# Kernel optimization log

Measured on AMD Instinct MI355X. Metric: run time of the kernel, lower is better.

## Reference

```python
import jax, jax.numpy as jnp
import numpy as np

DIM = 768
HEADS = 12
HEAD_DIM = DIM // HEADS


def setup_inputs() -> dict:
    key = jax.random.key(0)
    ks = jax.random.split(key, 5)
    B, S = 4, 2048
    init = 0.02
    x = jax.random.normal(ks[0], (B, S, DIM), dtype=jnp.float32)
    w_qkv = jax.random.normal(ks[1], (DIM, 3 * DIM), dtype=jnp.float32) * init
    b_qkv = jnp.zeros((3 * DIM,), dtype=jnp.float32)
    w_out = jax.random.normal(ks[2], (DIM, DIM), dtype=jnp.float32) * init
    b_out = jnp.zeros((DIM,), dtype=jnp.float32)
    return {"x": x, "w_qkv": w_qkv, "b_qkv": b_qkv, "w_out": w_out, "b_out": b_out}


def reference(x, w_qkv, b_qkv, w_out, b_out):
    B, S, D = x.shape
    # QKV projection: [B,S,3D] -> [3,B,H,S,hd]
    qkv = x @ w_qkv + b_qkv
    qkv = qkv.reshape(B, S, 3, HEADS, HEAD_DIM).transpose(2, 0, 3, 1, 4)
    q, k, v = qkv[0], qkv[1], qkv[2]
    # NOTE: original scales by 1/sqrt(head_num), not 1/sqrt(head_dim)
    scale = 1.0 / jnp.sqrt(jnp.float32(HEADS))
    scores = jnp.einsum("bhqd,bhkd->bhqk", q, k) * scale
    attn = jax.nn.softmax(scores, axis=-1)
    out = jnp.einsum("bhqk,bhkd->bhqd", attn, v)
    out = out.transpose(0, 2, 1, 3).reshape(B, S, D)
    return out @ w_out + b_out
```

## Files before the change

### kernel.cpp

```cpp
#include <hip/hip_runtime.h>
#include <hip/hip_bf16.h>
#include <cstdint>
#include <cstddef>

#define HEADS 12
#define HD    64
#define NB    4
#define SEQ   2048
#define DIM   768
#define NQKV  2304

static constexpr float QSCALE = 0.2886751345948129f * 1.4426950408889634f;

typedef __attribute__((ext_vector_type(8))) short short8;
typedef __attribute__((ext_vector_type(4))) short short4v;
typedef __attribute__((ext_vector_type(4))) float f32x4;

__device__ inline unsigned short f2bf(float x) {
    union { float f; uint32_t u; } v; v.f = x;
    return (unsigned short)((v.u + 0x7fffu + ((v.u >> 16) & 1u)) >> 16);
}

__device__ inline unsigned short f2bf_fast(float x) {
    __hip_bfloat16 h = __float2bfloat16(x);
    unsigned short u;
    __builtin_memcpy(&u, &h, 2);
    return u;
}

__device__ inline void gld16(const void* g, void* l) {
    __builtin_amdgcn_global_load_lds(
        (const __attribute__((address_space(1))) unsigned int*)g,
        (__attribute__((address_space(3))) unsigned int*)l, 16, 0, 0);
}

__global__ __launch_bounds__(256) void convert_x_kernel(
    const float* __restrict__ x, unsigned short* __restrict__ xb)
{
    const size_t i = ((size_t)blockIdx.x * 256 + threadIdx.x) * 8;
    const float4 a = *reinterpret_cast<const float4*>(x + i);
    const float4 b = *reinterpret_cast<const float4*>(x + i + 4);
    short8 o;
    o[0] = (short)f2bf(a.x); o[1] = (short)f2bf(a.y);
    o[2] = (short)f2bf(a.z); o[3] = (short)f2bf(a.w);
    o[4] = (short)f2bf(b.x); o[5] = (short)f2bf(b.y);
    o[6] = (short)f2bf(b.z); o[7] = (short)f2bf(b.w);
    *reinterpret_cast<short8*>(xb + i) = o;
}

__global__ __launch_bounds__(256) void transpose_w_kernel(
    const float* __restrict__ w, unsigned short* __restrict__ wT,
    int ncols , int nrows )
{
    __shared__ float tile[64][65];
    const int k0 = blockIdx.y * 64;
    const int n0 = blockIdx.x * 64;
    const int tr = threadIdx.x >> 4;
    const int tc4 = (threadIdx.x & 15) * 4;
    #pragma unroll
    for (int it = 0; it < 4; ++it) {
        const int kk = tr + it * 16;
        *reinterpret_cast<float4*>(&tile[kk][tc4]) =
            *reinterpret_cast<const float4*>(w + (size_t)(k0 + kk) * ncols + n0 + tc4);
    }
    __syncthreads();
    #pragma unroll
    for (int it = 0; it < 4; ++it) {
        const int nn = tr + it * 16;
        short4v o;
        #pragma unroll
        for (int r = 0; r < 4; ++r) o[r] = (short)f2bf(tile[tc4 + r][nn]);
        *reinterpret_cast<short4v*>(wT + (size_t)(n0 + nn) * nrows + k0 + tc4) = o;
    }
}

__global__ __launch_bounds__(256) void qkv_gemm_bf16(
    const unsigned short* __restrict__ A,
    const unsigned short* __restrict__ BT,
    const float* __restrict__ bias,
    unsigned short* __restrict__ qb, unsigned short* __restrict__ kb,
    unsigned short* __restrict__ vt)
{
    __shared__ __align__(16) unsigned short As[128][64];
    __shared__ __align__(16) unsigned short Bs[128][64];

    const int tid = threadIdx.x;
    const int wave = tid >> 6;
    const int lane = tid & 63;
    const int col = lane & 15;
    const int g = lane >> 4;
    const int m0 = blockIdx.y * 128;
    const int n0 = blockIdx.x * 128;
    const int wr = wave >> 1, wc = wave & 1;

    const int srow = tid >> 3;
    const int scl  = tid & 7;

    f32x4 acc[4][4] = {};

    for (int kt = 0; kt < DIM; kt += 64) {
        __syncthreads();
        #pragma unroll
        for (int it = 0; it < 4; ++it) {
            const int row = srow + it * 32;
            const int cg = scl ^ (row & 7);
            gld16(A + (size_t)(m0 + row) * DIM + kt + cg * 8,
                  &As[0][0] + (size_t)(it * 256 + wave * 64) * 8);
            gld16(BT + (size_t)(n0 + row) * DIM + kt + cg * 8,
                  &Bs[0][0] + (size_t)(it * 256 + wave * 64) * 8);
        }
        __syncthreads();

        #pragma unroll
        for (int ks = 0; ks < 2; ++ks) {
            short8 af[4], bf[4];
            #pragma unroll
            for (int i = 0; i < 4; ++i) {
                const int ra = wr * 64 + i * 16 + col;
                af[i] = *reinterpret_cast<const short8*>(
                    &As[ra][(((ks * 4 + g) ^ (ra & 7)) << 3)]);
                const int rb = wc * 64 + i * 16 + col;
                bf[i] = *reinterpret_cast<const short8*>(
                    &Bs[rb][(((ks * 4 + g) ^ (rb & 7)) << 3)]);
            }
            #pragma unroll
            for (int i = 0; i < 4; ++i)
                #pragma unroll
                for (int j = 0; j < 4; ++j)
                    acc[i][j] = __builtin_amdgcn_mfma_f32_16x16x32_bf16(
                        af[i], bf[j], acc[i][j], 0, 0, 0);
        }
    }

    const int which = n0 / DIM;
    #pragma unroll
    for (int j = 0; j < 4; ++j) {
        const int n = n0 + wc * 64 + j * 16 + col;
        const int rem = n - which * DIM;
        const int h = rem >> 6, dh = rem & 63;
        const float bj = bias[n];
        #pragma unroll
        for (int i = 0; i < 4; ++i) {
            const int mbase = m0 + wr * 64 + i * 16 + g * 4;
            const int b_ = mbase >> 11;
            const int s_ = mbase & 2047;
            const size_t bh = (size_t)(b_ * HEADS + h);
            if (which == 2) {
                short4v pk;
                #pragma unroll
                for (int r = 0; r < 4; ++r)
                    pk[r] = (short)f2bf(acc[i][j][r] + bj);
                *reinterpret_cast<short4v*>(vt + (bh * HD + dh) * SEQ + s_) = pk;
            } else {
                unsigned short* dst = (which == 0) ? qb : kb;
                const float sc = (which == 0) ? QSCALE : 1.0f;
                #pragma unroll
                for (int r = 0; r < 4; ++r)
                    dst[(bh * SEQ + s_ + r) * HD + dh] =
                        f2bf((acc[i][j][r] + bj) * sc);
            }
        }
    }
}

__global__ __launch_bounds__(512) void attn_kernel(
    const unsigned short* __restrict__ qb, const unsigned short* __restrict__ kbuf,
    const unsigned short* __restrict__ vt, unsigned short* __restrict__ ctxb)
{
    __shared__ __align__(16) unsigned short Ks[2][64][64];
    __shared__ __align__(16) unsigned short Vs[2][64][64];
    __shared__ __align__(16) unsigned short Ps[8][16][64];

    const int tid = threadIdx.x;
    const int wave = tid >> 6;
    const int lane = tid & 63;
    const int col = lane & 15;
    const int g   = lane >> 4;

    const int bid = blockIdx.x;
    const int vbid = (bid & 7) * 96 + (bid >> 3);
    const int bh = vbid >> 4;
    const int q0 = (vbid & 15) * 128;
    const int wq = q0 + wave * 16 + col;

    const size_t hb = (size_t)bh * SEQ * HD;

    short8 qf[2];
    {
        const unsigned short* src = qb + hb + (size_t)wq * HD + g * 8;
        qf[0] = *reinterpret_cast<const short8*>(src);
        qf[1] = *reinterpret_cast<const short8*>(src + 32);
    }

    f32x4 acc4[4] = {};
    float l_part = 0.0f;

    const unsigned short* Kg = kbuf + hb;
    const unsigned short* Vg = vt + hb;

    const int srow = tid >> 3;
    const int scl  = tid & 7;
    const int scg  = scl ^ (srow & 7);

    auto STAGE = [&](int jt, int bsel) {
        const int kb0 = jt * 64;
        gld16(Kg + (size_t)(kb0 + srow) * HD + scg * 8,
              &Ks[bsel][0][0] + (size_t)tid * 8);
        gld16(Vg + (size_t)srow * SEQ + kb0 + scg * 8,
              &Vs[bsel][0][0] + (size_t)tid * 8);
    };

    const int NT = SEQ / 64;
    STAGE(0, 0);

    for (int jt = 0; jt < NT; ++jt) {
        const int cur = jt & 1;
        if (jt + 1 < NT) {
            STAGE(jt + 1, cur ^ 1);
            asm volatile("s_waitcnt vmcnt(2)" ::: "memory");
        } else {
            asm volatile("s_waitcnt vmcnt(0)" ::: "memory");
        }
        __builtin_amdgcn_s_barrier();

        f32x4 st[4] = {};
        __builtin_amdgcn_s_setprio(1);
        #pragma unroll
        for (int m = 0; m < 4; ++m) {
            const int row = m * 16 + col;
            const short8 kf0 = *reinterpret_cast<const short8*>(
                &Ks[cur][row][((g ^ (row & 7)) << 3)]);
            const short8 kf1 = *reinterpret_cast<const short8*>(
                &Ks[cur][row][(((g + 4) ^ (row & 7)) << 3)]);
            st[m] = __builtin_amdgcn_mfma_f32_16x16x32_bf16(kf0, qf[0], st[m], 0, 0, 0);
            st[m] = __builtin_amdgcn_mfma_f32_16x16x32_bf16(kf1, qf[1], st[m], 0, 0, 0);
        }
        __builtin_amdgcn_s_setprio(0);

        float s0 = 0.0f, s1 = 0.0f, s2 = 0.0f, s3 = 0.0f;
        #pragma unroll
        for (int m = 0; m < 4; ++m) {
            float p[4];
            p[0] = __builtin_amdgcn_exp2f(st[m][0]);
            p[1] = __builtin_amdgcn_exp2f(st[m][1]);
            p[2] = __builtin_amdgcn_exp2f(st[m][2]);
            p[3] = __builtin_amdgcn_exp2f(st[m][3]);
            s0 += p[0]; s1 += p[1]; s2 += p[2]; s3 += p[3];
            short4v pk;
            #pragma unroll
            for (int r = 0; r < 4; ++r) pk[r] = (short)f2bf_fast(p[r]);
            const int scw = (2 * m + (g >> 1)) ^ (col & 7);
            *reinterpret_cast<short4v*>(
                &Ps[wave][col][(scw << 3) + ((g & 1) << 2)]) = pk;
        }
        l_part += (s0 + s1) + (s2 + s3);

        const short8 pf0 = *reinterpret_cast<const short8*>(
            &Ps[wave][col][((g ^ (col & 7)) << 3)]);
        const short8 pf1 = *reinterpret_cast<const short8*>(
            &Ps[wave][col][(((g + 4) ^ (col & 7)) << 3)]);

        __builtin_amdgcn_s_setprio(1);
        #pragma unroll
        for (int nb = 0; nb < 4; ++nb) {
            const int row = nb * 16 + col;
            const short8 vf0 = *reinterpret_cast<const short8*>(
                &Vs[cur][row][((g ^ (row & 7)) << 3)]);
            const short8 vf1 = *reinterpret_cast<const short8*>(
                &Vs[cur][row][(((g + 4) ^ (row & 7)) << 3)]);
            acc4[nb] = __builtin_amdgcn_mfma_f32_16x16x32_bf16(pf0, vf0, acc4[nb], 0, 0, 0);
            acc4[nb] = __builtin_amdgcn_mfma_f32_16x16x32_bf16(pf1, vf1, acc4[nb], 0, 0, 0);
        }
        __builtin_amdgcn_s_setprio(0);

        __builtin_amdgcn_s_barrier();
    }

    float lt = l_part + __shfl_xor(l_part, 16);
    lt += __shfl_xor(lt, 32);
    float lr[4];
    #pragma unroll
    for (int r = 0; r < 4; ++r) lr[r] = 1.0f / __shfl(lt, g * 4 + r);
    const int b_ = bh / HEADS;
    const int h = bh - b_ * HEADS;
    #pragma unroll
    for (int nb = 0; nb < 4; ++nb)
        #pragma unroll
        for (int r = 0; r < 4; ++r) {
            const int s_ = q0 + wave * 16 + g * 4 + r;
            ctxb[((size_t)b_ * SEQ + s_) * DIM + h * HD + nb * 16 + col] =
                f2bf_fast(acc4[nb][r] * lr[r]);
        }
}

__global__ __launch_bounds__(256) void out_gemm_bf16(
    const unsigned short* __restrict__ A,
    const unsigned short* __restrict__ BT,
    const float* __restrict__ bias, float* __restrict__ out)
{
    __shared__ __align__(16) unsigned short As[128][64];
    __shared__ __align__(16) unsigned short Bs[128][64];

    const int tid = threadIdx.x;
    const int wave = tid >> 6;
    const int lane = tid & 63;
    const int col = lane & 15;
    const int g = lane >> 4;
    const int m0 = blockIdx.y * 128;
    const int n0 = blockIdx.x * 128;
    const int wr = wave >> 1, wc = wave & 1;

    const int srow = tid >> 3;
    const int scl  = tid & 7;

    f32x4 acc[4][4] = {};

    for (int kt = 0; kt < DIM; kt += 64) {
        __syncthreads();
        #pragma unroll
        for (int it = 0; it < 4; ++it) {
            const int row = srow + it * 32;
            const int cg = scl ^ (row & 7);
            gld16(A + (size_t)(m0 + row) * DIM + kt + cg * 8,
                  &As[0][0] + (size_t)(it * 256 + wave * 64) * 8);
            gld16(BT + (size_t)(n0 + row) * DIM + kt + cg * 8,
                  &Bs[0][0] + (size_t)(it * 256 + wave * 64) * 8);
        }
        __syncthreads();

        #pragma unroll
        for (int ks = 0; ks < 2; ++ks) {
            short8 af[4], bf[4];
            #pragma unroll
            for (int i = 0; i < 4; ++i) {
                const int ra = wr * 64 + i * 16 + col;
                af[i] = *reinterpret_cast<const short8*>(
                    &As[ra][(((ks * 4 + g) ^ (ra & 7)) << 3)]);
                const int rb = wc * 64 + i * 16 + col;
                bf[i] = *reinterpret_cast<const short8*>(
                    &Bs[rb][(((ks * 4 + g) ^ (rb & 7)) << 3)]);
            }
            #pragma unroll
            for (int i = 0; i < 4; ++i)
                #pragma unroll
                for (int j = 0; j < 4; ++j)
                    acc[i][j] = __builtin_amdgcn_mfma_f32_16x16x32_bf16(
                        af[i], bf[j], acc[i][j], 0, 0, 0);
        }
    }

    #pragma unroll
    for (int j = 0; j < 4; ++j) {
        const int n = n0 + wc * 64 + j * 16 + col;
        const float bj = bias[n];
        #pragma unroll
        for (int i = 0; i < 4; ++i) {
            const int m = m0 + wr * 64 + i * 16 + g * 4;
            #pragma unroll
            for (int r = 0; r < 4; ++r)
                out[(size_t)(m + r) * DIM + n] = acc[i][j][r] + bj;
        }
    }
}

extern "C" void kernel_launch(void* const* d_in, const int* in_sizes, int n_in,
                              void* d_out, int out_size, void* d_ws, size_t ws_size,
                              hipStream_t stream)
{
    const float* x     = (const float*)d_in[0];
    const float* w_qkv = (const float*)d_in[1];
    const float* b_qkv = (const float*)d_in[2];
    const float* w_out = (const float*)d_in[3];
    const float* b_out = (const float*)d_in[4];
    float* out = (float*)d_out;

    const size_t QSZ = (size_t)NB * HEADS * SEQ * HD;
    unsigned short* qb   = (unsigned short*)d_ws;
    unsigned short* kb   = qb + QSZ;
    unsigned short* vt   = kb + QSZ;
    unsigned short* xb   = vt + QSZ;
    unsigned short* ctxb = xb + QSZ;
    unsigned short* wqT  = ctxb + QSZ;
    unsigned short* woT  = wqT + (size_t)NQKV * DIM;

    convert_x_kernel<<<3072, 256, 0, stream>>>(x, xb);
    transpose_w_kernel<<<dim3(NQKV / 64, DIM / 64), 256, 0, stream>>>(
        w_qkv, wqT, NQKV, DIM);
    transpose_w_kernel<<<dim3(DIM / 64, DIM / 64), 256, 0, stream>>>(
        w_out, woT, DIM, DIM);

    qkv_gemm_bf16<<<dim3(NQKV / 128, (NB * SEQ) / 128), 256, 0, stream>>>(
        xb, wqT, b_qkv, qb, kb, vt);
    attn_kernel<<<dim3((SEQ / 128) * NB * HEADS), 512, 0, stream>>>(qb, kb, vt, ctxb);
    out_gemm_bf16<<<dim3(DIM / 128, (NB * SEQ) / 128), 256, 0, stream>>>(
        ctxb, woT, b_out, out);
}
```

Baseline: 153.5 us.

## Double-buffer GEMM LDS tiles with 8 waves and merge prep kernels

Merges the x-conversion and two weight-transpose kernels into one launch to cut launch overhead. Both GEMMs move to 512-thread blocks with 8 waves each owning a 64x32 sub-tile, and use double-buffered LDS so the next K tile's global-to-LDS loads overlap the current tile's MFMAs. This halves per-wave register accumulators and leaves one barrier per K step, at the cost of doubled LDS per block and possibly lower occupancy.

Result: faster. 148.6 us (-3.2%).

```diff
diff --git a/kernel.cpp b/kernel.cpp
--- a/kernel.cpp
+++ b/kernel.cpp
@@ -34,27 +34,12 @@
         (__attribute__((address_space(3))) unsigned int*)l, 16, 0, 0);
 }
 
-__global__ __launch_bounds__(256) void convert_x_kernel(
-    const float* __restrict__ x, unsigned short* __restrict__ xb)
-{
-    const size_t i = ((size_t)blockIdx.x * 256 + threadIdx.x) * 8;
-    const float4 a = *reinterpret_cast<const float4*>(x + i);
-    const float4 b = *reinterpret_cast<const float4*>(x + i + 4);
-    short8 o;
-    o[0] = (short)f2bf(a.x); o[1] = (short)f2bf(a.y);
-    o[2] = (short)f2bf(a.z); o[3] = (short)f2bf(a.w);
-    o[4] = (short)f2bf(b.x); o[5] = (short)f2bf(b.y);
-    o[6] = (short)f2bf(b.z); o[7] = (short)f2bf(b.w);
-    *reinterpret_cast<short8*>(xb + i) = o;
-}
-
-__global__ __launch_bounds__(256) void transpose_w_kernel(
+__device__ inline void transpose_tile(
     const float* __restrict__ w, unsigned short* __restrict__ wT,
-    int ncols , int nrows )
-{
-    __shared__ float tile[64][65];
-    const int k0 = blockIdx.y * 64;
-    const int n0 = blockIdx.x * 64;
+    int ncols, int nrows, int bx, int by, float (*tile)[65])
+{
+    const int k0 = by * 64;
+    const int n0 = bx * 64;
     const int tr = threadIdx.x >> 4;
     const int tc4 = (threadIdx.x & 15) * 4;
     #pragma unroll
@@ -74,15 +59,41 @@
     }
 }
 
-__global__ __launch_bounds__(256) void qkv_gemm_bf16(
+__global__ __launch_bounds__(256) void prep_kernel(
+    const float* __restrict__ x, unsigned short* __restrict__ xb,
+    const float* __restrict__ wq, unsigned short* __restrict__ wqT,
+    const float* __restrict__ wo, unsigned short* __restrict__ woT)
+{
+    __shared__ float tile[64][65];
+    const int bid = blockIdx.x;
+    if (bid < 3072) {
+        const size_t i = ((size_t)bid * 256 + threadIdx.x) * 8;
+        const float4 a = *reinterpret_cast<const float4*>(x + i);
+        const float4 b = *reinterpret_cast<const float4*>(x + i + 4);
+        short8 o;
+        o[0] = (short)f2bf(a.x); o[1] = (short)f2bf(a.y);
+        o[2] = (short)f2bf(a.z); o[3] = (short)f2bf(a.w);
+        o[4] = (short)f2bf(b.x); o[5] = (short)f2bf(b.y);
+        o[6] = (short)f2bf(b.z); o[7] = (short)f2bf(b.w);
+        *reinterpret_cast<short8*>(xb + i) = o;
+    } else if (bid < 3072 + 432) {
+        const int r = bid - 3072;
+        transpose_tile(wq, wqT, NQKV, DIM, r % 36, r / 36, tile);
+    } else {
+        const int r = bid - 3504;
+        transpose_tile(wo, woT, DIM, DIM, r % 12, r / 12, tile);
+    }
+}
+
+__global__ __launch_bounds__(512) void qkv_gemm_bf16(
     const unsigned short* __restrict__ A,
     const unsigned short* __restrict__ BT,
     const float* __restrict__ bias,
     unsigned short* __restrict__ qb, unsigned short* __restrict__ kb,
     unsigned short* __restrict__ vt)
 {
-    __shared__ __align__(16) unsigned short As[128][64];
-    __shared__ __align__(16) unsigned short Bs[128][64];
+    __shared__ __align__(16) unsigned short As[2][128][64];
+    __shared__ __align__(16) unsigned short Bs[2][128][64];
 
     const int tid = threadIdx.x;
     const int wave = tid >> 6;
@@ -91,51 +102,66 @@
     const int g = lane >> 4;
     const int m0 = blockIdx.y * 128;
     const int n0 = blockIdx.x * 128;
-    const int wr = wave >> 1, wc = wave & 1;
-
-    const int srow = tid >> 3;
-    const int scl  = tid & 7;
-
-    f32x4 acc[4][4] = {};
-
-    for (int kt = 0; kt < DIM; kt += 64) {
-        __syncthreads();
-        #pragma unroll
-        for (int it = 0; it < 4; ++it) {
-            const int row = srow + it * 32;
-            const int cg = scl ^ (row & 7);
+    const int wr = wave >> 2;
+    const int wc = wave & 3;
+
+    f32x4 acc[4][2] = {};
+
+    auto STAGE = [&](int kt, int bsel) {
+        #pragma unroll
+        for (int it = 0; it < 2; ++it) {
+            const int slot = tid + it * 512;
+            const int row = slot >> 3;
+            const int cg = (slot & 7) ^ (row & 7);
             gld16(A + (size_t)(m0 + row) * DIM + kt + cg * 8,
-                  &As[0][0] + (size_t)(it * 256 + wave * 64) * 8);
+                  &As[bsel][0][0] + (size_t)slot * 8);
             gld16(BT + (size_t)(n0 + row) * DIM + kt + cg * 8,
-                  &Bs[0][0] + (size_t)(it * 256 + wave * 64) * 8);
-        }
-        __syncthreads();
+                  &Bs[bsel][0][0] + (size_t)slot * 8);
+        }
+    };
+
+    const int NKT = DIM / 64;
+    STAGE(0, 0);
+    asm volatile("s_waitcnt vmcnt(0)" ::: "memory");
+    __builtin_amdgcn_s_barrier();
+
+    for (int t = 0; t < NKT; ++t) {
+        const int cur = t & 1;
+        if (t + 1 < NKT) STAGE((t + 1) * 64, cur ^ 1);
 
         #pragma unroll
         for (int ks = 0; ks < 2; ++ks) {
-            short8 af[4], bf[4];
+            short8 af[4], bf[2];
             #pragma unroll
             for (int i = 0; i < 4; ++i) {
                 const int ra = wr * 64 + i * 16 + col;
                 af[i] = *reinterpret_cast<const short8*>(
-                    &As[ra][(((ks * 4 + g) ^ (ra & 7)) << 3)]);
-                const int rb = wc * 64 + i * 16 + col;
-                bf[i] = *reinterpret_cast<const short8*>(
-                    &Bs[rb][(((ks * 4 + g) ^ (rb & 7)) << 3)]);
+                    &As[cur][ra][(((ks * 4 + g) ^ (ra & 7)) << 3)]);
+            }
+            #pragma unroll
+            for (int j = 0; j < 2; ++j) {
+                const int rb = wc * 32 + j * 16 + col;
+                bf[j] = *reinterpret_cast<const short8*>(
+                    &Bs[cur][rb][(((ks * 4 + g) ^ (rb & 7)) << 3)]);
             }
             #pragma unroll
             for (int i = 0; i < 4; ++i)
                 #pragma unroll
-                for (int j = 0; j < 4; ++j)
+                for (int j = 0; j < 2; ++j)
                     acc[i][j] = __builtin_amdgcn_mfma_f32_16x16x32_bf16(
                         af[i], bf[j], acc[i][j], 0, 0, 0);
         }
+
+        if (t + 1 < NKT) {
+            asm volatile("s_waitcnt vmcnt(0)" ::: "memory");
+            __builtin_amdgcn_s_barrier();
+        }
     }
 
     const int which = n0 / DIM;
     #pragma unroll
-    for (int j = 0; j < 4; ++j) {
-        const int n = n0 + wc * 64 + j * 16 + col;
+    for (int j = 0; j < 2; ++j) {
+        const int n = n0 + wc * 32 + j * 16 + col;
         const int rem = n - which * DIM;
         const int h = rem >> 6, dh = rem & 63;
         const float bj = bias[n];
@@ -293,13 +319,13 @@
         }
 }
 
-__global__ __launch_bounds__(256) void out_gemm_bf16(
+__global__ __launch_bounds__(512) void out_gemm_bf16(
     const unsigned short* __restrict__ A,
     const unsigned short* __restrict__ BT,
     const float* __restrict__ bias, float* __restrict__ out)
 {
-    __shared__ __align__(16) unsigned short As[128][64];
-    __shared__ __align__(16) unsigned short Bs[128][64];
+    __shared__ __align__(16) unsigned short As[2][128][64];
+    __shared__ __align__(16) unsigned short Bs[2][128][64];
 
     const int tid = threadIdx.x;
     const int wave = tid >> 6;
@@ -308,50 +334,65 @@
     const int g = lane >> 4;
     const int m0 = blockIdx.y * 128;
     const int n0 = blockIdx.x * 128;
-    const int wr = wave >> 1, wc = wave & 1;
-
-    const int srow = tid >> 3;
-    const int scl  = tid & 7;
-
-    f32x4 acc[4][4] = {};
-
-    for (int kt = 0; kt < DIM; kt += 64) {
-        __syncthreads();
-        #pragma unroll
-        for (int it = 0; it < 4; ++it) {
-            const int row = srow + it * 32;
-            const int cg = scl ^ (row & 7);
+    const int wr = wave >> 2;
+    const int wc = wave & 3;
+
+    f32x4 acc[4][2] = {};
+
+    auto STAGE = [&](int kt, int bsel) {
+        #pragma unroll
+        for (int it = 0; it < 2; ++it) {
+            const int slot = tid + it * 512;
+            const int row = slot >> 3;
+            const int cg = (slot & 7) ^ (row & 7);
             gld16(A + (size_t)(m0 + row) * DIM + kt + cg * 8,
-                  &As[0][0] + (size_t)(it * 256 + wave * 64) * 8);
+                  &As[bsel][0][0] + (size_t)slot * 8);
             gld16(BT + (size_t)(n0 + row) * DIM + kt + cg * 8,
-                  &Bs[0][0] + (size_t)(it * 256 + wave * 64) * 8);
-        }
-        __syncthreads();
+                  &Bs[bsel][0][0] + (size_t)slot * 8);
+        }
+    };
+
+    const int NKT = DIM / 64;
+    STAGE(0, 0);
+    asm volatile("s_waitcnt vmcnt(0)" ::: "memory");
+    __builtin_amdgcn_s_barrier();
+
+    for (int t = 0; t < NKT; ++t) {
+        const int cur = t & 1;
+        if (t + 1 < NKT) STAGE((t + 1) * 64, cur ^ 1);
 
         #pragma unroll
         for (int ks = 0; ks < 2; ++ks) {
-            short8 af[4], bf[4];
+            short8 af[4], bf[2];
             #pragma unroll
             for (int i = 0; i < 4; ++i) {
                 const int ra = wr * 64 + i * 16 + col;
                 af[i] = *reinterpret_cast<const short8*>(
-                    &As[ra][(((ks * 4 + g) ^ (ra & 7)) << 3)]);
-                const int rb = wc * 64 + i * 16 + col;
-                bf[i] = *reinterpret_cast<const short8*>(
-                    &Bs[rb][(((ks * 4 + g) ^ (rb & 7)) << 3)]);
+                    &As[cur][ra][(((ks * 4 + g) ^ (ra & 7)) << 3)]);
+            }
+            #pragma unroll
+            for (int j = 0; j < 2; ++j) {
+                const int rb = wc * 32 + j * 16 + col;
+                bf[j] = *reinterpret_cast<const short8*>(
+                    &Bs[cur][rb][(((ks * 4 + g) ^ (rb & 7)) << 3)]);
             }
             #pragma unroll
             for (int i = 0; i < 4; ++i)
                 #pragma unroll
-                for (int j = 0; j < 4; ++j)
+                for (int j = 0; j < 2; ++j)
                     acc[i][j] = __builtin_amdgcn_mfma_f32_16x16x32_bf16(
                         af[i], bf[j], acc[i][j], 0, 0, 0);
         }
-    }
-
-    #pragma unroll
-    for (int j = 0; j < 4; ++j) {
-        const int n = n0 + wc * 64 + j * 16 + col;
+
+        if (t + 1 < NKT) {
+            asm volatile("s_waitcnt vmcnt(0)" ::: "memory");
+            __builtin_amdgcn_s_barrier();
+        }
+    }
+
+    #pragma unroll
+    for (int j = 0; j < 2; ++j) {
+        const int n = n0 + wc * 32 + j * 16 + col;
         const float bj = bias[n];
         #pragma unroll
         for (int i = 0; i < 4; ++i) {
@@ -383,15 +424,10 @@
     unsigned short* wqT  = ctxb + QSZ;
     unsigned short* woT  = wqT + (size_t)NQKV * DIM;
 
-    convert_x_kernel<<<3072, 256, 0, stream>>>(x, xb);
-    transpose_w_kernel<<<dim3(NQKV / 64, DIM / 64), 256, 0, stream>>>(
-        w_qkv, wqT, NQKV, DIM);
-    transpose_w_kernel<<<dim3(DIM / 64, DIM / 64), 256, 0, stream>>>(
-        w_out, woT, DIM, DIM);
-
-    qkv_gemm_bf16<<<dim3(NQKV / 128, (NB * SEQ) / 128), 256, 0, stream>>>(
+    prep_kernel<<<3648, 256, 0, stream>>>(x, xb, w_qkv, wqT, w_out, woT);
+    qkv_gemm_bf16<<<dim3(NQKV / 128, (NB * SEQ) / 128), 512, 0, stream>>>(
         xb, wqT, b_qkv, qb, kb, vt);
     attn_kernel<<<dim3((SEQ / 128) * NB * HEADS), 512, 0, stream>>>(qb, kb, vt, ctxb);
-    out_gemm_bf16<<<dim3(DIM / 128, (NB * SEQ) / 128), 256, 0, stream>>>(
+    out_gemm_bf16<<<dim3(DIM / 128, (NB * SEQ) / 128), 512, 0, stream>>>(
         ctxb, woT, b_out, out);
 }
```
